# Kernel optimization log

Measured on AMD Instinct MI355X. Metric: run time of the kernel, lower is better.

The kernel has to match this reference:

```python
import jax, jax.numpy as jnp
import numpy as np

B, T_PREFIX, C_IN = 8, 6144, 8
OUT_LEN, OUT_C = 2048, 8
AUX_DIM = 16
D_MODEL, D_STATE, HEADDIM, EXPAND = 256, 32, 64, 2
D_INNER = EXPAND * D_MODEL            # 512
NHEADS = D_INNER // HEADDIM           # 8
CONV_DIM = D_INNER + 2 * D_STATE      # 576
D_PROJ = 2 * D_INNER + 2 * D_STATE + NHEADS  # 1096
N_LAYERS = 2
CHUNK = 64
PATCH = 16
PRECONV_K = 5
DCONV_K = 4


def setup_inputs() -> dict:
    key = jax.random.key(0)
    ks = iter(jax.random.split(key, 64))
    def rn(shape, s=0.02):
        return s * jax.random.normal(next(ks), shape, jnp.float32)
    inp = dict(
        x_prefix=jax.random.normal(next(ks), (B, T_PREFIX, C_IN), jnp.float32),
        y_aux=jax.random.normal(next(ks), (B, AUX_DIM), jnp.float32),
        pre_conv_w=rn((D_MODEL, C_IN, PRECONV_K), 0.1),
        pre_conv_b=rn((D_MODEL,)),
        patch_w=rn((D_MODEL, D_MODEL, PATCH), 0.05),
        patch_b=rn((D_MODEL,)),
        mask_token=rn((D_MODEL,)),
        aux_w=rn((AUX_DIM, D_MODEL), 0.1),
        aux_b=rn((D_MODEL,)),
        patch_out_w=rn((2 * D_MODEL, OUT_C * PATCH), 0.05),
        patch_out_b=rn((OUT_C * PATCH,)),
    )
    for d in ('fwd', 'bwd'):
        inp[f'{d}_norm_w'] = jnp.ones((N_LAYERS, D_MODEL), jnp.float32)
        inp[f'{d}_inproj'] = rn((N_LAYERS, D_MODEL, D_PROJ), 0.05)
        inp[f'{d}_conv_w'] = rn((N_LAYERS, CONV_DIM, DCONV_K), 0.2)
        inp[f'{d}_conv_b'] = rn((N_LAYERS, CONV_DIM))
        inp[f'{d}_dtbias'] = rn((N_LAYERS, NHEADS), 0.5)
        inp[f'{d}_Alog'] = jnp.tile(jnp.log(jnp.arange(1, NHEADS + 1, dtype=jnp.float32)), (N_LAYERS, 1))
        inp[f'{d}_D'] = jnp.ones((N_LAYERS, NHEADS), jnp.float32)
        inp[f'{d}_gnorm'] = jnp.ones((N_LAYERS, D_INNER), jnp.float32)
        inp[f'{d}_outproj'] = rn((N_LAYERS, D_INNER, D_MODEL), 0.05)
    return inp


def rmsnorm(x, w, eps=1e-5):
    return x * jax.lax.rsqrt(jnp.mean(x * x, axis=-1, keepdims=True) + eps) * w


def conv1d(x, w, b, stride, pad):  # x: [B,C,T], w: [O,I,K]
    y = jax.lax.conv_general_dilated(x, w, (stride,), [(pad, pad)],
                                     dimension_numbers=('NCH', 'OIH', 'NCH'))
    return y + b[None, :, None]


def mamba_block(u, inproj, conv_w, conv_b, dtbias, Alog, Dp, gnorm_w, outproj):
    # Mamba-2/SSD style block: in_proj -> z | xBC | dt, causal depthwise conv,
    # selective scan with per-head scalar decay A, +D skip, gated RMSNorm, out_proj.
    b, T, _ = u.shape
    zxbcdt = u @ inproj                                   # [b,T,D_PROJ]
    z = zxbcdt[..., :D_INNER]
    xBC = zxbcdt[..., D_INNER:D_INNER + CONV_DIM]
    dt = jax.nn.softplus(zxbcdt[..., -NHEADS:] + dtbias)  # [b,T,H]
    # causal depthwise conv over time
    xc = jax.lax.conv_general_dilated(xBC.transpose(0, 2, 1), conv_w[:, None, :], (1,),
                                      [(DCONV_K - 1, 0)],
                                      dimension_numbers=('NCH', 'OIH', 'NCH'),
                                      feature_group_count=CONV_DIM)
    xBC = jax.nn.silu((xc + conv_b[None, :, None]).transpose(0, 2, 1))
    xs = xBC[..., :D_INNER].reshape(b, T, NHEADS, HEADDIM)  # [b,T,H,P]
    Bm = xBC[..., D_INNER:D_INNER + D_STATE]                # [b,T,N]
    Cm = xBC[..., D_INNER + D_STATE:]                       # [b,T,N]
    A = -jnp.exp(Alog)                                      # [H]

    def step(h, inps):  # h: [b,H,P,N]
        dt_t, x_t, B_t, C_t = inps
        dA = jnp.exp(dt_t * A)[:, :, None, None]
        h = h * dA + (dt_t[:, :, None] * x_t)[..., None] * B_t[:, None, None, :]
        y = jnp.einsum('bhpn,bn->bhp', h, C_t)
        return h, y

    h0 = jnp.zeros((b, NHEADS, HEADDIM, D_STATE), u.dtype)
    _, ys = jax.lax.scan(step, h0, (dt.transpose(1, 0, 2), xs.transpose(1, 0, 2, 3),
                                    Bm.transpose(1, 0, 2), Cm.transpose(1, 0, 2)))
    y = ys.transpose(1, 0, 2, 3) + Dp[None, None, :, None] * xs
    y = y.reshape(b, T, D_INNER)
    y = rmsnorm(y * jax.nn.silu(z), gnorm_w)
    return y @ outproj


def reference(x_prefix, y_aux, pre_conv_w, pre_conv_b, patch_w, patch_b, mask_token,
              aux_w, aux_b, fwd_norm_w, fwd_inproj, fwd_conv_w, fwd_conv_b, fwd_dtbias,
              fwd_Alog, fwd_D, fwd_gnorm, fwd_outproj, bwd_norm_w, bwd_inproj,
              bwd_conv_w, bwd_conv_b, bwd_dtbias, bwd_Alog, bwd_D, bwd_gnorm,
              bwd_outproj, patch_out_w, patch_out_b):
    b = x_prefix.shape[0]
    t_total = T_PREFIX + OUT_LEN
    x_full = jnp.pad(x_prefix, ((0, 0), (0, OUT_LEN), (0, 0)))        # zeros for future
    x = jax.nn.silu(conv1d(x_full.transpose(0, 2, 1), pre_conv_w, pre_conv_b, 1, PRECONV_K // 2))
    x = conv1d(x, patch_w, patch_b, PATCH, 0).transpose(0, 2, 1)      # [b, n_tokens, d_model]
    n_tokens = x.shape[1]
    # eval mode: deterministic future-patch mask, dropout is identity
    starts = jnp.arange(n_tokens) * PATCH
    mask = (starts >= T_PREFIX)[None, :, None]
    x = jnp.where(mask, mask_token[None, None, :], x)
    aux_bias = jax.nn.silu(y_aux @ aux_w + aux_b)[:, None, :]
    x = x + aux_bias
    pad_t = (-n_tokens) % CHUNK
    if pad_t:
        x = jnp.pad(x, ((0, 0), (0, pad_t), (0, 0)))
    h_f = x
    h_b = x[:, ::-1]
    for i in range(N_LAYERS):
        h_f = h_f + mamba_block(rmsnorm(h_f, fwd_norm_w[i]), fwd_inproj[i], fwd_conv_w[i],
                                fwd_conv_b[i], fwd_dtbias[i], fwd_Alog[i], fwd_D[i],
                                fwd_gnorm[i], fwd_outproj[i])
        h_b = h_b + mamba_block(rmsnorm(h_b, bwd_norm_w[i]), bwd_inproj[i], bwd_conv_w[i],
                                bwd_conv_b[i], bwd_dtbias[i], bwd_Alog[i], bwd_D[i],
                                bwd_gnorm[i], bwd_outproj[i])
    h = jnp.concatenate([h_f, h_b[:, ::-1]], axis=-1)[:, :n_tokens]   # [b,n,2*d_model]
    patch_pred = h @ patch_out_w + patch_out_b                        # [b,n,out_c*patch]
    y = patch_pred.reshape(b, n_tokens, OUT_C, PATCH).reshape(b, n_tokens * PATCH, OUT_C)
    y = y[:, :t_total, :]
    return y[:, T_PREFIX:, :]
```

## Files before the change

kernel.cpp:

```cpp
#include <hip/hip_runtime.h>
#include <hip/hip_bf16.h>
#include <math.h>

#define BSZ      8
#define TPREF    6144
#define CIN      8
#define DMODEL   256
#define DINNER   512
#define DSTATE   32
#define NHEADS   8
#define HEADDIM  64
#define CONVDIM  576
#define DPROJ    1096
#define ZXW      1088
#define NTOK     512
#define NVIS     384
#define TBWD     128
#define MFWD     (BSZ * NTOK)
#define MBWD     (BSZ * TBWD)
#define MALL     (MFWD + MBWD)

typedef float f32x4 __attribute__((ext_vector_type(4)));
typedef __bf16 bf16x8 __attribute__((ext_vector_type(8)));

__device__ __forceinline__ float silu_f(float x) { return x / (1.f + expf(-x)); }

#define ASYNC16(gp, lp) \
    __builtin_amdgcn_global_load_lds((const __attribute__((address_space(1))) void*)(gp), \
                                     (__attribute__((address_space(3))) void*)(lp), 16, 0, 0)

__global__ __launch_bounds__(256) void gemm_mfma(
    const __bf16* __restrict__ A, const __bf16* __restrict__ Bt,
    float* __restrict__ C, const float* __restrict__ bias,
    int N, int K, int ldc, int flags) {
    __shared__ char sm[16384];
    int tid = threadIdx.x;
    int m0 = blockIdx.y * 128, n0 = blockIdx.x * 128;
    int klen = K / gridDim.z;
    int kbeg = blockIdx.z * klen;
    int w = tid >> 6, l = tid & 63;
    int wm = w >> 1, wn = w & 1;
    int lm = l & 15, q = l >> 4;

    f32x4 acc[4][4];
    #pragma unroll
    for (int i = 0; i < 4; i++)
        #pragma unroll
        for (int j = 0; j < 4; j++) acc[i][j] = (f32x4)0.f;

    for (int k0 = 0; k0 < klen; k0 += 32) {
        int kb = kbeg + k0;
        #pragma unroll
        for (int i = 0; i < 2; i++) {
            int s = i * 256 + tid;
            ASYNC16(A + (size_t)(m0 + (s >> 2)) * K + kb + (s & 3) * 8, sm + s * 16);
        }
        #pragma unroll
        for (int i = 0; i < 2; i++) {
            int s = i * 256 + tid;
            ASYNC16(Bt + (size_t)(n0 + (s >> 2)) * K + kb + (s & 3) * 8, sm + 8192 + s * 16);
        }
        __syncthreads();
        bf16x8 af[4], bfr[4];
        #pragma unroll
        for (int mf = 0; mf < 4; mf++)
            af[mf] = *(const bf16x8*)(sm + (wm * 64 + mf * 16 + lm) * 64 + q * 16);
        #pragma unroll
        for (int nf = 0; nf < 4; nf++)
            bfr[nf] = *(const bf16x8*)(sm + 8192 + (wn * 64 + nf * 16 + lm) * 64 + q * 16);
        #pragma unroll
        for (int mf = 0; mf < 4; mf++)
            #pragma unroll
            for (int nf = 0; nf < 4; nf++)
                acc[mf][nf] = __builtin_amdgcn_mfma_f32_16x16x32_bf16(af[mf], bfr[nf], acc[mf][nf], 0, 0, 0);
        __syncthreads();
    }

    #pragma unroll
    for (int mf = 0; mf < 4; mf++) {
        int mbase = m0 + wm * 64 + mf * 16 + q * 4;
        #pragma unroll
        for (int nf = 0; nf < 4; nf++) {
            int n = n0 + wn * 64 + nf * 16 + lm;
            if (n < N) {
                #pragma unroll
                for (int r = 0; r < 4; r++) {
                    float v = acc[mf][nf][r];
                    if (flags & 4) {
                        v = silu_f(v + bias[n]);
                        ((__bf16*)C)[(size_t)(mbase + r) * ldc + n] = (__bf16)v;
                    } else if (flags & 16) {
                        int mm = mbase + r;
                        int bb = mm / NVIS, tk = mm - bb * NVIS;
                        atomicAdd(C + ((size_t)(bb * NTOK + tk)) * 256 + n, v);
                    } else if (flags & 2) {
                        atomicAdd(C + (size_t)(mbase + r) * ldc + n, v);
                    } else {
                        C[(size_t)(mbase + r) * ldc + n] = v;
                    }
                }
            }
        }
    }
}

__global__ __launch_bounds__(256) void preconv_gemm(
    const float* __restrict__ xp, const __bf16* __restrict__ WpreT,
    const float* __restrict__ bias, __bf16* __restrict__ Apatch) {
    __shared__ char sm[32768];
    int tid = threadIdx.x;
    int m0 = blockIdx.y * 128, n0 = blockIdx.x * 128;
    int w = tid >> 6, l = tid & 63;
    int wm = w >> 1, wn = w & 1, lm = l & 15, q = l >> 4;

    #pragma unroll
    for (int i = 0; i < 4; i++) {
        int s = i * 256 + tid;
        int kh = s >> 9, row = (s & 511) >> 2, within = s & 3;
        ASYNC16(WpreT + (size_t)(n0 + row) * 64 + kh * 32 + within * 8, sm + 16384 + s * 16);
    }
    if (tid < 128) {
        int m = m0 + tid;
        int b = m / TPREF, t = m - b * TPREF;
        __bf16 d[64];
        #pragma unroll
        for (int j = 40; j < 64; j++) d[j] = (__bf16)0.f;
        #pragma unroll
        for (int k = 0; k < 5; k++) {
            int tt = t - 2 + k;
            bool ok = (tt >= 0) && (tt < TPREF);
            const float* s = xp + ((size_t)b * TPREF + tt) * 8;
            #pragma unroll
            for (int i = 0; i < 8; i++)
                d[i * 5 + k] = ok ? (__bf16)s[i] : (__bf16)0.f;
        }
        uint4* o0 = (uint4*)(sm + tid * 64);
        uint4* o1 = (uint4*)(sm + 8192 + tid * 64);
        #pragma unroll
        for (int k = 0; k < 4; k++) { o0[k] = ((const uint4*)d)[k]; o1[k] = ((const uint4*)d)[4 + k]; }
    }
    __syncthreads();

    f32x4 acc[4][4];
    #pragma unroll
    for (int i = 0; i < 4; i++)
        #pragma unroll
        for (int j = 0; j < 4; j++) acc[i][j] = (f32x4)0.f;
    #pragma unroll
    for (int kh = 0; kh < 2; kh++) {
        bf16x8 af[4], bfr[4];
        #pragma unroll
        for (int mf = 0; mf < 4; mf++)
            af[mf] = *(const bf16x8*)(sm + kh * 8192 + (wm * 64 + mf * 16 + lm) * 64 + q * 16);
        #pragma unroll
        for (int nf = 0; nf < 4; nf++)
            bfr[nf] = *(const bf16x8*)(sm + 16384 + kh * 8192 + (wn * 64 + nf * 16 + lm) * 64 + q * 16);
        #pragma unroll
        for (int mf = 0; mf < 4; mf++)
            #pragma unroll
            for (int nf = 0; nf < 4; nf++)
                acc[mf][nf] = __builtin_amdgcn_mfma_f32_16x16x32_bf16(af[mf], bfr[nf], acc[mf][nf], 0, 0, 0);
    }
    #pragma unroll
    for (int mf = 0; mf < 4; mf++) {
        int mbase = m0 + wm * 64 + mf * 16 + q * 4;
        #pragma unroll
        for (int nf = 0; nf < 4; nf++) {
            int n = n0 + wn * 64 + nf * 16 + lm;
            #pragma unroll
            for (int r = 0; r < 4; r++) {
                float v = silu_f(acc[mf][nf][r] + bias[n]);
                Apatch[(size_t)(mbase + r) * 256 + n] = (__bf16)v;
            }
        }
    }
}

__global__ __launch_bounds__(256) void final_gemm(
    const float* __restrict__ h_all, const __bf16* __restrict__ poT,
    float* __restrict__ out) {
    __shared__ __bf16 Asm_[128][40];
    __shared__ char Bsm[8192];
    int tid = threadIdx.x;
    int m0 = blockIdx.y * 128;
    int z = blockIdx.z;
    int dir = z >> 1, kh = z & 1;
    int koff = kh * 128;
    int w = tid >> 6, l = tid & 63;
    int wm = w >> 1, wn_ = w & 1, lm = l & 15, q = l >> 4;
    f32x4 acc[4][4];
    #pragma unroll
    for (int i = 0; i < 4; i++)
        #pragma unroll
        for (int j = 0; j < 4; j++) acc[i][j] = (f32x4)0.f;

    int r = tid >> 1, half = tid & 1;
    int m = m0 + r;
    int b = m >> 7, jj = m & 127;
    size_t arow = (dir == 0) ? ((size_t)(b * NTOK + NVIS + jj) * 256)
                             : ((size_t)MFWD * 256 + (size_t)(b * TBWD + (TBWD - 1 - jj)) * 256);
    for (int k0 = 0; k0 < 128; k0 += 32) {
        {
            const float4* sp = (const float4*)(h_all + arow + koff + k0 + half * 16);
            float4 v0 = sp[0], v1 = sp[1], v2 = sp[2], v3 = sp[3];
            union { uint4 u; __bf16 hh[8]; } d0, d1;
            d0.hh[0] = (__bf16)v0.x; d0.hh[1] = (__bf16)v0.y; d0.hh[2] = (__bf16)v0.z; d0.hh[3] = (__bf16)v0.w;
            d0.hh[4] = (__bf16)v1.x; d0.hh[5] = (__bf16)v1.y; d0.hh[6] = (__bf16)v1.z; d0.hh[7] = (__bf16)v1.w;
            d1.hh[0] = (__bf16)v2.x; d1.hh[1] = (__bf16)v2.y; d1.hh[2] = (__bf16)v2.z; d1.hh[3] = (__bf16)v2.w;
            d1.hh[4] = (__bf16)v3.x; d1.hh[5] = (__bf16)v3.y; d1.hh[6] = (__bf16)v3.z; d1.hh[7] = (__bf16)v3.w;
            *(uint4*)&Asm_[r][half * 16] = d0.u;
            *(uint4*)&Asm_[r][half * 16 + 8] = d1.u;
        }
        #pragma unroll
        for (int i = 0; i < 2; i++) {
            int s = i * 256 + tid;
            ASYNC16(poT + (size_t)(s >> 2) * 512 + dir * 256 + koff + k0 + (s & 3) * 8, Bsm + s * 16);
        }
        __syncthreads();
        bf16x8 af[4], bfr[4];
        #pragma unroll
        for (int mf = 0; mf < 4; mf++)
            af[mf] = *(const bf16x8*)&Asm_[wm * 64 + mf * 16 + lm][q * 8];
        #pragma unroll
        for (int nf = 0; nf < 4; nf++)
            bfr[nf] = *(const bf16x8*)(Bsm + (wn_ * 64 + nf * 16 + lm) * 64 + q * 16);
        #pragma unroll
        for (int mf = 0; mf < 4; mf++)
            #pragma unroll
            for (int nf = 0; nf < 4; nf++)
                acc[mf][nf] = __builtin_amdgcn_mfma_f32_16x16x32_bf16(af[mf], bfr[nf], acc[mf][nf], 0, 0, 0);
        __syncthreads();
    }
    #pragma unroll
    for (int mf = 0; mf < 4; mf++) {
        int mbase = m0 + wm * 64 + mf * 16 + q * 4;
        #pragma unroll
        for (int nf = 0; nf < 4; nf++) {
            int n = wn_ * 64 + nf * 16 + lm;
            #pragma unroll
            for (int rr = 0; rr < 4; rr++)
                atomicAdd(out + (size_t)(mbase + rr) * 128 + n, acc[mf][nf][rr]);
        }
    }
}

__global__ __launch_bounds__(256) void gemm_inproj(
    const __bf16* __restrict__ u, const __bf16* __restrict__ ipTf,
    const __bf16* __restrict__ ipTb, __bf16* __restrict__ zxb, float* __restrict__ dtc) {
    __shared__ char sm[16384];
    int tid = threadIdx.x;
    int m0 = blockIdx.y * 128, n0 = blockIdx.x * 128;
    const __bf16* Bt = (m0 >= MFWD) ? ipTb : ipTf;
    int w = tid >> 6, l = tid & 63;
    int wm = w >> 1, wn = w & 1, lm = l & 15, q = l >> 4;
    f32x4 acc[4][4];
    #pragma unroll
    for (int i = 0; i < 4; i++)
        #pragma unroll
        for (int j = 0; j < 4; j++) acc[i][j] = (f32x4)0.f;
    for (int k0 = 0; k0 < 256; k0 += 32) {
        #pragma unroll
        for (int i = 0; i < 2; i++) {
            int s = i * 256 + tid;
            ASYNC16(u + (size_t)(m0 + (s >> 2)) * 256 + k0 + (s & 3) * 8, sm + s * 16);
        }
        #pragma unroll
        for (int i = 0; i < 2; i++) {
            int s = i * 256 + tid;
            ASYNC16(Bt + (size_t)(n0 + (s >> 2)) * 256 + k0 + (s & 3) * 8, sm + 8192 + s * 16);
        }
        __syncthreads();
        bf16x8 af[4], bfr[4];
        #pragma unroll
        for (int mf = 0; mf < 4; mf++)
            af[mf] = *(const bf16x8*)(sm + (wm * 64 + mf * 16 + lm) * 64 + q * 16);
        #pragma unroll
        for (int nf = 0; nf < 4; nf++)
            bfr[nf] = *(const bf16x8*)(sm + 8192 + (wn * 64 + nf * 16 + lm) * 64 + q * 16);
        #pragma unroll
        for (int mf = 0; mf < 4; mf++)
            #pragma unroll
            for (int nf = 0; nf < 4; nf++)
                acc[mf][nf] = __builtin_amdgcn_mfma_f32_16x16x32_bf16(af[mf], bfr[nf], acc[mf][nf], 0, 0, 0);
        __syncthreads();
    }
    #pragma unroll
    for (int mf = 0; mf < 4; mf++) {
        int mbase = m0 + wm * 64 + mf * 16 + q * 4;
        #pragma unroll
        for (int nf = 0; nf < 4; nf++) {
            int n = n0 + wn * 64 + nf * 16 + lm;
            #pragma unroll
            for (int r = 0; r < 4; r++) {
                float v = acc[mf][nf][r];
                if (n < ZXW) zxb[(size_t)(mbase + r) * ZXW + n] = (__bf16)v;
                else if (n < DPROJ) dtc[(size_t)(mbase + r) * 8 + (n - ZXW)] = v;
            }
        }
    }
}

__global__ __launch_bounds__(256) void gemm_outproj(
    const __bf16* __restrict__ y2, const __bf16* __restrict__ opTf,
    const __bf16* __restrict__ opTb, float* __restrict__ C, int layer) {
    __shared__ char sm[16384];
    int tid = threadIdx.x;
    int yb = blockIdx.y;
    int m0 = (layer == 0) ? yb * 128
                          : ((yb < 8) ? (yb * 512 + 384) : (MFWD + (yb - 8) * 128));
    int n0 = blockIdx.x * 128;
    const __bf16* Bt = (m0 >= MFWD) ? opTb : opTf;
    int w = tid >> 6, l = tid & 63;
    int wm = w >> 1, wn = w & 1, lm = l & 15, q = l >> 4;
    f32x4 acc[4][4];
    #pragma unroll
    for (int i = 0; i < 4; i++)
        #pragma unroll
        for (int j = 0; j < 4; j++) acc[i][j] = (f32x4)0.f;
    for (int k0 = 0; k0 < 512; k0 += 32) {
        #pragma unroll
        for (int i = 0; i < 2; i++) {
            int s = i * 256 + tid;
            ASYNC16(y2 + (size_t)(m0 + (s >> 2)) * 512 + k0 + (s & 3) * 8, sm + s * 16);
        }
        #pragma unroll
        for (int i = 0; i < 2; i++) {
            int s = i * 256 + tid;
            ASYNC16(Bt + (size_t)(n0 + (s >> 2)) * 512 + k0 + (s & 3) * 8, sm + 8192 + s * 16);
        }
        __syncthreads();
        bf16x8 af[4], bfr[4];
        #pragma unroll
        for (int mf = 0; mf < 4; mf++)
            af[mf] = *(const bf16x8*)(sm + (wm * 64 + mf * 16 + lm) * 64 + q * 16);
        #pragma unroll
        for (int nf = 0; nf < 4; nf++)
            bfr[nf] = *(const bf16x8*)(sm + 8192 + (wn * 64 + nf * 16 + lm) * 64 + q * 16);
        #pragma unroll
        for (int mf = 0; mf < 4; mf++)
            #pragma unroll
            for (int nf = 0; nf < 4; nf++)
                acc[mf][nf] = __builtin_amdgcn_mfma_f32_16x16x32_bf16(af[mf], bfr[nf], acc[mf][nf], 0, 0, 0);
        __syncthreads();
    }
    #pragma unroll
    for (int mf = 0; mf < 4; mf++) {
        int mbase = m0 + wm * 64 + mf * 16 + q * 4;
        #pragma unroll
        for (int nf = 0; nf < 4; nf++) {
            int n = n0 + wn * 64 + nf * 16 + lm;
            #pragma unroll
            for (int r = 0; r < 4; r++) {
                size_t ci = (size_t)(mbase + r) * DMODEL + n;
                C[ci] += acc[mf][nf][r];
            }
        }
    }
}

__global__ __launch_bounds__(256) void rmsnorm_all(
    const float* __restrict__ h, const float* __restrict__ wf,
    const float* __restrict__ wb, __bf16* __restrict__ u) {
    int row = blockIdx.x * 4 + (threadIdx.x >> 6);
    int lane = threadIdx.x & 63;
    const float* w = (row >= MFWD) ? wb : wf;
    float4 v = ((const float4*)(h + (size_t)row * 256))[lane];
    float ss = v.x * v.x + v.y * v.y + v.z * v.z + v.w * v.w;
    #pragma unroll
    for (int off = 32; off >= 1; off >>= 1) ss += __shfl_xor(ss, off);
    float rs = rsqrtf(ss * (1.f / 256.f) + 1e-5f);
    float4 wv = ((const float4*)w)[lane];
    __bf16 o4[4] = {(__bf16)(v.x * rs * wv.x), (__bf16)(v.y * rs * wv.y),
                    (__bf16)(v.z * rs * wv.z), (__bf16)(v.w * rs * wv.w)};
    *(uint2*)(u + (size_t)row * 256 + lane * 4) = *(uint2*)o4;
}

__global__ __launch_bounds__(256) void gatednorm_all(
    const __bf16* __restrict__ ysD, const __bf16* __restrict__ zxb,
    const float* __restrict__ gwf, const float* __restrict__ gwb,
    __bf16* __restrict__ y2) {
    int row = blockIdx.x * 4 + (threadIdx.x >> 6);
    int lane = threadIdx.x & 63;
    const float* gw = (row >= MFWD) ? gwb : gwf;
    union { uint4 u; __bf16 hh[8]; } yv, zv;
    yv.u = *(const uint4*)(ysD + (size_t)row * 512 + lane * 8);
    zv.u = *(const uint4*)(zxb + (size_t)row * ZXW + lane * 8);
    float g[8];
    #pragma unroll
    for (int j = 0; j < 8; j++) g[j] = (float)yv.hh[j] * silu_f((float)zv.hh[j]);
    float ss = 0.f;
    #pragma unroll
    for (int j = 0; j < 8; j++) ss += g[j] * g[j];
    #pragma unroll
    for (int off = 32; off >= 1; off >>= 1) ss += __shfl_xor(ss, off);
    float rs = rsqrtf(ss * (1.f / 512.f) + 1e-5f);
    const float4* gr = (const float4*)(gw + lane * 8);
    float4 g0 = gr[0], g1 = gr[1];
    union { uint4 u; __bf16 hh[8]; } d;
    d.hh[0] = (__bf16)(g[0] * rs * g0.x); d.hh[1] = (__bf16)(g[1] * rs * g0.y);
    d.hh[2] = (__bf16)(g[2] * rs * g0.z); d.hh[3] = (__bf16)(g[3] * rs * g0.w);
    d.hh[4] = (__bf16)(g[4] * rs * g1.x); d.hh[5] = (__bf16)(g[5] * rs * g1.y);
    d.hh[6] = (__bf16)(g[6] * rs * g1.z); d.hh[7] = (__bf16)(g[7] * rs * g1.w);
    *(uint4*)(y2 + (size_t)row * 512 + lane * 8) = d.u;
}

__global__ void prep_all(const float* __restrict__ pre_conv_w, const float* __restrict__ patch_w,
                         const float* __restrict__ ip0, const float* __restrict__ ip1,
                         const float* __restrict__ op0, const float* __restrict__ op1,
                         const float* __restrict__ pow_, const float* __restrict__ pob,
                         const float* __restrict__ y_aux, const float* __restrict__ aux_w,
                         const float* __restrict__ aux_b,
                         const float* __restrict__ patch_b, const float* __restrict__ mtok,
                         __bf16* __restrict__ WpreT, __bf16* __restrict__ WtT,
                         __bf16* __restrict__ inprojT, __bf16* __restrict__ outprojT,
                         __bf16* __restrict__ poT, float* __restrict__ dout,
                         float* __restrict__ h_all) {
    __shared__ float tile[32][33];
    int bx = blockIdx.x, tid = threadIdx.x;
    int tx = tid & 31, ty = tid >> 5;
    if (bx < 256) {
        int o = bx, c = tid;
        float f[16];
        const float4* s = (const float4*)(patch_w + (size_t)o * 4096 + c * 16);
        #pragma unroll
        for (int j = 0; j < 4; j++) *(float4*)&f[j * 4] = s[j];
        #pragma unroll
        for (int k = 0; k < 16; k++)
            WtT[(size_t)o * 4096 + k * 256 + c] = (__bf16)f[k];
        return;
    }
    bx -= 256;
    if (bx < 1152) {
        int seg = bx / 288, rem = bx % 288;
        int n0 = (rem / 8) * 32, k0 = (rem % 8) * 32;
        const float* src = (seg < 2 ? ip0 : ip1) + (size_t)(seg & 1) * 256 * DPROJ;
        #pragma unroll
        for (int j = 0; j < 4; j++) {
            int r = ty + j * 8;
            int n = n0 + tx;
            tile[r][tx] = (n < DPROJ) ? src[(size_t)(k0 + r) * DPROJ + n] : 0.f;
        }
        __syncthreads();
        __bf16* dst = inprojT + (size_t)seg * 1152 * 256;
        #pragma unroll
        for (int j = 0; j < 4; j++) {
            int r = ty + j * 8;
            dst[(size_t)(n0 + r) * 256 + k0 + tx] = (__bf16)tile[tx][r];
        }
        return;
    }
    bx -= 1152;
    if (bx < 512) {
        int s = bx / 128, rem = bx % 128;
        int n0 = (rem / 16) * 32, k0 = (rem % 16) * 32;
        const float* src = (s < 2 ? op0 : op1) + (size_t)(s & 1) * DINNER * DMODEL;
        #pragma unroll
        for (int j = 0; j < 4; j++) {
            int r = ty + j * 8;
            tile[r][tx] = src[(size_t)(k0 + r) * 256 + n0 + tx];
        }
        __syncthreads();
        __bf16* dst = outprojT + (size_t)s * 256 * 512;
        #pragma unroll
        for (int j = 0; j < 4; j++) {
            int r = ty + j * 8;
            dst[(size_t)(n0 + r) * 512 + k0 + tx] = (__bf16)tile[tx][r];
        }
        return;
    }
    bx -= 512;
    if (bx < 64) {
        int n0 = (bx / 16) * 32, k0 = (bx % 16) * 32;
        #pragma unroll
        for (int j = 0; j < 4; j++) {
            int r = ty + j * 8;
            tile[r][tx] = pow_[(size_t)(k0 + r) * 128 + n0 + tx];
        }
        __syncthreads();
        #pragma unroll
        for (int j = 0; j < 4; j++) {
            int r = ty + j * 8;
            poT[(size_t)(n0 + r) * 512 + k0 + tx] = (__bf16)tile[tx][r];
        }
        return;
    }
    bx -= 64;
    if (bx < 64) {
        int idx = bx * 256 + tid;
        int o = idx >> 6, kk = idx & 63;
        WpreT[idx] = (kk < 40) ? (__bf16)pre_conv_w[o * 40 + kk] : (__bf16)0.f;
        return;
    }
    bx -= 64;
    if (bx < 512) {
        int idx = bx * 256 + tid;
        dout[idx] = pob[idx & 127];
        return;
    }
    bx -= 512;
    {
        int row = bx, o = tid;
        int b; bool masked;
        if (row < MFWD) { b = row >> 9; int tok = row & 511; masked = (tok >= NVIS); }
        else { b = (row - MFWD) >> 7; masked = true; }
        float acc = aux_b[o];
        #pragma unroll
        for (int i = 0; i < 16; i++) acc += y_aux[b * 16 + i] * aux_w[i * 256 + o];
        float v = (masked ? mtok[o] : patch_b[o]) + silu_f(acc);
        h_all[(size_t)row * 256 + o] = v;
    }
}

__global__ __launch_bounds__(256) void scan_local(
    const __bf16* __restrict__ zxb,
    const float* __restrict__ cwf, const float* __restrict__ cbf,
    const float* __restrict__ cwb, const float* __restrict__ cbb,
    const float* __restrict__ dtc,
    const float* __restrict__ dtbf, const float* __restrict__ dtbb,
    const float* __restrict__ Alogf, const float* __restrict__ Alogb,
    const float* __restrict__ Dpf, const float* __restrict__ Dpb,
    __bf16* __restrict__ ysD,
    __bf16* __restrict__ ChatF, __bf16* __restrict__ ChatB,
    float* __restrict__ dSF, float* __restrict__ dSB,
    float* __restrict__ DcsF, float* __restrict__ DcsB, int layer) {
    int id = blockIdx.x, hd = blockIdx.y;
    int b, c, T, NC; size_t rowbase;
    __bf16* Chat; float *dS, *Dcs;
    const float *dtb, *Alog, *Dp, *cw, *cb;
    if (id < 64) { b = id >> 3; c = id & 7; T = NTOK; NC = 8; rowbase = (size_t)b * NTOK;
                   Chat = ChatF; dS = dSF; Dcs = DcsF;
                   dtb = dtbf; Alog = Alogf; Dp = Dpf; cw = cwf; cb = cbf; }
    else { int i2 = id - 64; b = i2 >> 1; c = i2 & 1; T = TBWD; NC = 2;
           rowbase = (size_t)MFWD + (size_t)b * TBWD;
           Chat = ChatB; dS = dSB; Dcs = DcsB;
           dtb = dtbb; Alog = Alogb; Dp = Dpb; cw = cwb; cb = cbb; }
    bool skipY = (layer == 1) && (id < 64) && (c < 6);
    int bh = b * 8 + hd;
    int t0 = c * 64;
    int tid = threadIdx.x;
    int w = tid >> 6, l = tid & 63;
    int lm = l & 15, q = l >> 4;
    float A = -expf(Alog[hd]);
    float Dh = Dp[hd];

    __shared__ char smem[40704];
    __bf16 (*Xl)[72]  = (__bf16(*)[72])(smem);
    __bf16 (*BCl)[72] = (__bf16(*)[72])(smem + 9216);
    __bf16 (*Pl)[72]  = (__bf16(*)[72])(smem + 9216);
    __bf16 (*Wbl)[72] = (__bf16(*)[72])(smem + 18432);
    float* lcs = (float*)(smem + 23040);
    float* dts = (float*)(smem + 23296);
    __bf16 (*xraw)[64] = (__bf16(*)[64])(smem + 23552);
    __bf16 (*braw)[64] = (__bf16(*)[64])(smem + 32128);

    for (int s = tid; s < 1072; s += 256) {
        int arr = (s >= 536) ? 1 : 0;
        int s2 = s - arr * 536;
        int r = s2 >> 3, seg = s2 & 7;
        int t = t0 - 3 + r;
        uint4 v = make_uint4(0u, 0u, 0u, 0u);
        if (t >= 0) {
            size_t col = arr ? (size_t)(1024 + seg * 8) : (size_t)(DINNER + hd * 64 + seg * 8);
            v = *(const uint4*)(zxb + (rowbase + t) * (size_t)ZXW + col);
        }
        if (arr) *(uint4*)&braw[r][seg * 8] = v;
        else     *(uint4*)&xraw[r][seg * 8] = v;
    }
    __syncthreads();

    {
        int cX = hd * 64 + l;
        float w0 = cw[cX * 4], w1 = cw[cX * 4 + 1], w2 = cw[cX * 4 + 2], w3 = cw[cX * 4 + 3];
        float cbv = cb[cX];
        int tb = w * 16;
        float a0 = (float)xraw[tb][l], a1 = (float)xraw[tb + 1][l], a2 = (float)xraw[tb + 2][l];
        union { uint4 u; __bf16 h[8]; } p0, p1;
        #pragma unroll
        for (int j = 0; j < 16; j++) {
            float a3 = (float)xraw[tb + j + 3][l];
            float acc = cbv + w0 * a0 + w1 * a1 + w2 * a2 + w3 * a3;
            if (j < 8) p0.h[j] = (__bf16)silu_f(acc);
            else       p1.h[j - 8] = (__bf16)silu_f(acc);
            a0 = a1; a1 = a2; a2 = a3;
        }
        *(uint4*)&Xl[l][tb]     = p0.u;
        *(uint4*)&Xl[l][tb + 8] = p1.u;
    }
    {
        int cc = 512 + l;
        float w0 = cw[cc * 4], w1 = cw[cc * 4 + 1], w2 = cw[cc * 4 + 2], w3 = cw[cc * 4 + 3];
        float cbv = cb[cc];
        int tb = w * 16;
        float a0 = (float)braw[tb][l], a1 = (float)braw[tb + 1][l], a2 = (float)braw[tb + 2][l];
        #pragma unroll
        for (int j = 0; j < 16; j++) {
            float a3 = (float)braw[tb + j + 3][l];
            float acc = cbv + w0 * a0 + w1 * a1 + w2 * a2 + w3 * a3;
            BCl[tb + j][l] = (__bf16)silu_f(acc);
            a0 = a1; a1 = a2; a2 = a3;
        }
    }
    float xdt = dtc[(rowbase + t0 + l) * 8 + hd] + dtb[hd];
    float dtv = (xdt > 20.f) ? xdt : log1pf(expf(xdt));
    float lc = A * dtv;
    #pragma unroll
    for (int off = 1; off < 64; off <<= 1) {
        float o = __shfl_up(lc, off);
        if (l >= off) lc += o;
    }
    float lc63 = __shfl(lc, 63);
    float wj = expf(lc63 - lc) * dtv;
    float eli = expf(lc);
    if (w == 0) {
        lcs[l] = lc; dts[l] = dtv;
        if (l == 0) Dcs[bh * NC + c] = expf(lc63);
    }
    __syncthreads();

    if (!skipY) {
        union { uint4 u; __bf16 h[8]; } s, d;
        s.u = *(const uint4*)&BCl[l][32 + w * 8];
        #pragma unroll
        for (int j = 0; j < 8; j++) d.h[j] = (__bf16)(eli * (float)s.h[j]);
        *(uint4*)(Chat + ((size_t)(bh * NC + c) * 64 + l) * 32 + w * 8) = d.u;
    }
    {
        union { uint4 u; __bf16 h[8]; } s;
        s.u = *(const uint4*)&BCl[l][w * 8];
        #pragma unroll
        for (int j = 0; j < 8; j++) Wbl[w * 8 + j][l] = (__bf16)(wj * (float)s.h[j]);
    }
    bf16x8 cfr, bfr[4];
    if (!skipY) {
        cfr = *(const bf16x8*)&BCl[w * 16 + lm][32 + q * 8];
        #pragma unroll
        for (int tj = 0; tj < 4; tj++)
            if (tj <= w) bfr[tj] = *(const bf16x8*)&BCl[tj * 16 + lm][q * 8];
    }
    __syncthreads();

    if (!skipY) {
        float lci[4];
        #pragma unroll
        for (int r = 0; r < 4; r++) lci[r] = lcs[w * 16 + q * 4 + r];
        #pragma unroll
        for (int tj = 0; tj < 4; tj++) {
            if (tj > w) {
                #pragma unroll
                for (int r = 0; r < 4; r++) Pl[w * 16 + q * 4 + r][tj * 16 + lm] = (__bf16)0.f;
                continue;
            }
            f32x4 g = __builtin_amdgcn_mfma_f32_16x16x32_bf16(cfr, bfr[tj], (f32x4)0.f, 0, 0, 0);
            int j = tj * 16 + lm;
            float lcj = lcs[j], dtj = dts[j];
            #pragma unroll
            for (int r = 0; r < 4; r++) {
                int i = w * 16 + q * 4 + r;
                float v = (j <= i) ? g[r] * expf(lci[r] - lcj) * dtj : 0.f;
                if (j == i) v += Dh;
                Pl[i][j] = (__bf16)v;
            }
        }
    }
    __syncthreads();

    bf16x8 xf0[4], xf1[4];
    #pragma unroll
    for (int t4 = 0; t4 < 4; t4++) {
        xf0[t4] = *(const bf16x8*)&Xl[t4 * 16 + lm][q * 8];
        xf1[t4] = *(const bf16x8*)&Xl[t4 * 16 + lm][32 + q * 8];
    }
    if (!skipY) {
        bf16x8 pf0 = *(const bf16x8*)&Pl[w * 16 + lm][q * 8];
        bf16x8 pf1 = *(const bf16x8*)&Pl[w * 16 + lm][32 + q * 8];
        #pragma unroll
        for (int tp = 0; tp < 4; tp++) {
            f32x4 y = __builtin_amdgcn_mfma_f32_16x16x32_bf16(pf0, xf0[tp], (f32x4)0.f, 0, 0, 0);
            y = __builtin_amdgcn_mfma_f32_16x16x32_bf16(pf1, xf1[tp], y, 0, 0, 0);
            #pragma unroll
            for (int r = 0; r < 4; r++) {
                int i = w * 16 + q * 4 + r;
                ysD[(rowbase + t0 + i) * DINNER + hd * 64 + tp * 16 + lm] = (__bf16)y[r];
            }
        }
    }
    bf16x8 wf0[2], wf1[2];
    #pragma unroll
    for (int tn = 0; tn < 2; tn++) {
        wf0[tn] = *(const bf16x8*)&Wbl[tn * 16 + lm][q * 8];
        wf1[tn] = *(const bf16x8*)&Wbl[tn * 16 + lm][32 + q * 8];
    }
    float* dso = dS + (size_t)(bh * NC + c) * 2048;
    #pragma unroll
    for (int tn = 0; tn < 2; tn++) {
        f32x4 s = __builtin_amdgcn_mfma_f32_16x16x32_bf16(xf0[w], wf0[tn], (f32x4)0.f, 0, 0, 0);
        s = __builtin_amdgcn_mfma_f32_16x16x32_bf16(xf1[w], wf1[tn], s, 0, 0, 0);
        #pragma unroll
        for (int r = 0; r < 4; r++) {
            int pp = w * 16 + q * 4 + r, nn = tn * 16 + lm;
            dso[pp * 32 + nn] = s[r];
        }
    }
}

__global__ __launch_bounds__(256) void scan_tail(
    const float* __restrict__ dSF, const float* __restrict__ dSB,
    const float* __restrict__ DcsF, const float* __restrict__ DcsB,
    const __bf16* __restrict__ ChatF, const __bf16* __restrict__ ChatB,
    __bf16* __restrict__ ysD, int layer) {
    int blk = blockIdx.x;
    int dir = blk >= 64;
    int bh = blk & 63;
    int NC = dir ? 2 : 8;
    int T = dir ? TBWD : NTOK;
    int b = bh >> 3, hd = bh & 7;
    size_t rowbase = dir ? ((size_t)MFWD + (size_t)b * TBWD) : ((size_t)b * NTOK);
    const float* dS = dir ? dSB : dSF;
    const float* Dcs = dir ? DcsB : DcsF;
    const __bf16* Chat = dir ? ChatB : ChatF;
    int cmin = (layer == 1 && !dir) ? 6 : 1;
    int tid = threadIdx.x;
    __shared__ __bf16 Spl[8][64][40];
    {
        int p = tid >> 2, n0 = (tid & 3) * 8;
        float S[8];
        #pragma unroll
        for (int j = 0; j < 8; j++) S[j] = 0.f;
        for (int c = 0; c < NC; c++) {
            union { uint4 u; __bf16 hh[8]; } o;
            #pragma unroll
            for (int j = 0; j < 8; j++) o.hh[j] = (__bf16)S[j];
            *(uint4*)&Spl[c][p][n0] = o.u;
            float Dc = Dcs[bh * NC + c];
            const float4* dp = (const float4*)(dS + ((size_t)(bh * NC + c)) * 2048 + tid * 8);
            float4 d0 = dp[0], d1 = dp[1];
            S[0] = Dc * S[0] + d0.x; S[1] = Dc * S[1] + d0.y;
            S[2] = Dc * S[2] + d0.z; S[3] = Dc * S[3] + d0.w;
            S[4] = Dc * S[4] + d1.x; S[5] = Dc * S[5] + d1.y;
            S[6] = Dc * S[6] + d1.z; S[7] = Dc * S[7] + d1.w;
        }
    }
    __syncthreads();
    int w = tid >> 6, l = tid & 63, lm = l & 15, q = l >> 4;
    for (int c = cmin + w; c < NC; c += 4) {
        int t0 = c * 64;
        const __bf16* Cb = Chat + (size_t)(bh * NC + c) * 2048;
        bf16x8 cf[4], sf[4];
        #pragma unroll
        for (int t4 = 0; t4 < 4; t4++) {
            cf[t4] = *(const bf16x8*)(Cb + (t4 * 16 + lm) * 32 + q * 8);
            sf[t4] = *(const bf16x8*)&Spl[c][t4 * 16 + lm][q * 8];
        }
        #pragma unroll
        for (int ti = 0; ti < 4; ti++) {
            #pragma unroll
            for (int tp = 0; tp < 4; tp++) {
                f32x4 y = __builtin_amdgcn_mfma_f32_16x16x32_bf16(cf[ti], sf[tp], (f32x4)0.f, 0, 0, 0);
                #pragma unroll
                for (int r = 0; r < 4; r++) {
                    int i = ti * 16 + q * 4 + r;
                    size_t idx = (rowbase + t0 + i) * DINNER + hd * 64 + tp * 16 + lm;
                    ysD[idx] = (__bf16)((float)ysD[idx] + y[r]);
                }
            }
        }
    }
}

extern "C" void kernel_launch(void* const* d_in, const int* in_sizes, int n_in,
                              void* d_out, int out_size, void* d_ws, size_t ws_size,
                              hipStream_t stream) {
    const float* x_prefix    = (const float*)d_in[0];
    const float* y_aux       = (const float*)d_in[1];
    const float* pre_conv_w  = (const float*)d_in[2];
    const float* pre_conv_b  = (const float*)d_in[3];
    const float* patch_w     = (const float*)d_in[4];
    const float* patch_b     = (const float*)d_in[5];
    const float* mask_token  = (const float*)d_in[6];
    const float* aux_w       = (const float*)d_in[7];
    const float* aux_b       = (const float*)d_in[8];
    const float* patch_out_w = (const float*)d_in[9];
    const float* patch_out_b = (const float*)d_in[10];
    const float* w_norm[2]   = {(const float*)d_in[11], (const float*)d_in[20]};
    const float* w_inproj[2] = {(const float*)d_in[12], (const float*)d_in[21]};
    const float* w_convw[2]  = {(const float*)d_in[13], (const float*)d_in[22]};
    const float* w_convb[2]  = {(const float*)d_in[14], (const float*)d_in[23]};
    const float* w_dtb[2]    = {(const float*)d_in[15], (const float*)d_in[24]};
    const float* w_alog[2]   = {(const float*)d_in[16], (const float*)d_in[25]};
    const float* w_D[2]      = {(const float*)d_in[17], (const float*)d_in[26]};
    const float* w_gnorm[2]  = {(const float*)d_in[18], (const float*)d_in[27]};
    const float* w_outproj[2]= {(const float*)d_in[19], (const float*)d_in[28]};

    char* p = (char*)d_ws;
    auto alloc = [&](size_t bytes) { char* r = p; p += (bytes + 255) & ~255ULL; return r; };
    __bf16* A_patch  = (__bf16*)alloc((size_t)3072 * 4096 * 2);
    __bf16* WpreT    = (__bf16*)alloc((size_t)256 * 64 * 2);
    __bf16* WtT      = (__bf16*)alloc((size_t)256 * 4096 * 2);
    __bf16* inprojT  = (__bf16*)alloc((size_t)4 * 1152 * 256 * 2);
    __bf16* outprojT = (__bf16*)alloc((size_t)4 * 256 * 512 * 2);
    __bf16* poT      = (__bf16*)alloc((size_t)128 * 512 * 2);
    float*  h_all    = (float*)alloc((size_t)MALL * 256 * 4);
    __bf16* u        = (__bf16*)alloc((size_t)MALL * 256 * 2);
    __bf16* zxb      = (__bf16*)alloc((size_t)MALL * ZXW * 2);
    float*  dtc      = (float*)alloc((size_t)MALL * 8 * 4);
    __bf16* ysD      = (__bf16*)alloc((size_t)MALL * DINNER * 2);
    __bf16* y2       = (__bf16*)alloc((size_t)MALL * DINNER * 2);
    __bf16* ChatF    = (__bf16*)alloc((size_t)64 * 8 * 2048 * 2);
    __bf16* ChatB    = (__bf16*)alloc((size_t)64 * 2 * 2048 * 2);
    float*  dSF      = (float*)alloc((size_t)64 * 8 * 2048 * 4);
    float*  dSB      = (float*)alloc((size_t)64 * 2 * 2048 * 4);
    float*  DcsF     = (float*)alloc((size_t)64 * 8 * 4);
    float*  DcsB     = (float*)alloc((size_t)64 * 2 * 4);

    prep_all<<<256 + 1152 + 512 + 64 + 64 + 512 + MALL, 256, 0, stream>>>(
        pre_conv_w, patch_w, w_inproj[0], w_inproj[1], w_outproj[0], w_outproj[1],
        patch_out_w, patch_out_b, y_aux, aux_w, aux_b, patch_b, mask_token,
        WpreT, WtT, inprojT, outprojT, poT, (float*)d_out, h_all);
    preconv_gemm<<<dim3(2, (BSZ * TPREF) / 128), 256, 0, stream>>>(
        x_prefix, WpreT, pre_conv_b, A_patch);
    gemm_mfma<<<dim3(2, 24, 8), 256, 0, stream>>>(
        A_patch, WtT, h_all, nullptr, 256, 4096, 256, 16);

    for (int i = 0; i < 2; i++) {
        const __bf16* ipTf = inprojT + (size_t)(0 * 2 + i) * 1152 * 256;
        const __bf16* ipTb = inprojT + (size_t)(1 * 2 + i) * 1152 * 256;
        const __bf16* opTf = outprojT + (size_t)(0 * 2 + i) * 256 * 512;
        const __bf16* opTb = outprojT + (size_t)(1 * 2 + i) * 256 * 512;
        rmsnorm_all<<<MALL / 4, 256, 0, stream>>>(h_all, w_norm[0] + i * 256, w_norm[1] + i * 256, u);
        gemm_inproj<<<dim3(9, MALL / 128), 256, 0, stream>>>(u, ipTf, ipTb, zxb, dtc);
        scan_local<<<dim3(80, NHEADS), 256, 0, stream>>>(
            zxb,
            w_convw[0] + i * CONVDIM * 4, w_convb[0] + i * CONVDIM,
            w_convw[1] + i * CONVDIM * 4, w_convb[1] + i * CONVDIM,
            dtc,
            w_dtb[0] + i * 8, w_dtb[1] + i * 8,
            w_alog[0] + i * 8, w_alog[1] + i * 8,
            w_D[0] + i * 8, w_D[1] + i * 8,
            ysD, ChatF, ChatB, dSF, dSB, DcsF, DcsB, i);
        scan_tail<<<128, 256, 0, stream>>>(dSF, dSB, DcsF, DcsB, ChatF, ChatB, ysD, i);
        gatednorm_all<<<MALL / 4, 256, 0, stream>>>(
            ysD, zxb, w_gnorm[0] + i * DINNER, w_gnorm[1] + i * DINNER, y2);
        int oy = (i == 0) ? (MALL / 128) : 16;
        gemm_outproj<<<dim3(2, oy), 256, 0, stream>>>(y2, opTf, opTb, h_all, i);
    }

    final_gemm<<<dim3(1, 8, 4), 256, 0, stream>>>(h_all, poT, (float*)d_out);
}
```

Measured before the change: 323.3 us.

## Fuse RMSNorm and gated norm into in-proj and out-proj GEMM prologues

Removes the standalone rmsnorm_all and gatednorm_all kernels. Each GEMM now loads fp32 h (or ysD and z) directly, applies the weight and gating while staging the A tile into shared memory, and accumulates the row sum of squares. The per-row rsqrt scale is applied in the epilogue. This drops four launches per forward and the u/y2 intermediate round trips. The cost is that A-tile loads become synchronous register loads instead of async copies, and the norm work is redone by every column block: 9x for in-proj and 2x for out-proj.

```diff
diff --git a/kernel.cpp b/kernel.cpp
--- a/kernel.cpp
+++ b/kernel.cpp
@@ -245,12 +245,15 @@
 }
 
 __global__ __launch_bounds__(256) void gemm_inproj(
-    const __bf16* __restrict__ u, const __bf16* __restrict__ ipTf,
-    const __bf16* __restrict__ ipTb, __bf16* __restrict__ zxb, float* __restrict__ dtc) {
+    const float* __restrict__ h, const float* __restrict__ nwf, const float* __restrict__ nwb,
+    const __bf16* __restrict__ ipTf, const __bf16* __restrict__ ipTb,
+    __bf16* __restrict__ zxb, float* __restrict__ dtc) {
     __shared__ char sm[16384];
+    __shared__ float rsl[128];
     int tid = threadIdx.x;
     int m0 = blockIdx.y * 128, n0 = blockIdx.x * 128;
     const __bf16* Bt = (m0 >= MFWD) ? ipTb : ipTf;
+    const float* nw = (m0 >= MFWD) ? nwb : nwf;
     int w = tid >> 6, l = tid & 63;
     int wm = w >> 1, wn = w & 1, lm = l & 15, q = l >> 4;
     f32x4 acc[4][4];
@@ -258,11 +261,37 @@
     for (int i = 0; i < 4; i++)
         #pragma unroll
         for (int j = 0; j < 4; j++) acc[i][j] = (f32x4)0.f;
+
+    int ar = tid >> 1, aseg = tid & 1;
+    const float* hrow = h + (size_t)(m0 + ar) * 256;
+    float ss = 0.f;
+
     for (int k0 = 0; k0 < 256; k0 += 32) {
-        #pragma unroll
-        for (int i = 0; i < 2; i++) {
-            int s = i * 256 + tid;
-            ASYNC16(u + (size_t)(m0 + (s >> 2)) * 256 + k0 + (s & 3) * 8, sm + s * 16);
+        {
+            int cb = k0 + aseg * 16;
+            float4 v0 = *(const float4*)(hrow + cb);
+            float4 v1 = *(const float4*)(hrow + cb + 4);
+            float4 v2 = *(const float4*)(hrow + cb + 8);
+            float4 v3 = *(const float4*)(hrow + cb + 12);
+            float4 w0 = *(const float4*)(nw + cb);
+            float4 w1 = *(const float4*)(nw + cb + 4);
+            float4 w2 = *(const float4*)(nw + cb + 8);
+            float4 w3 = *(const float4*)(nw + cb + 12);
+            ss += v0.x * v0.x + v0.y * v0.y + v0.z * v0.z + v0.w * v0.w
+                + v1.x * v1.x + v1.y * v1.y + v1.z * v1.z + v1.w * v1.w
+                + v2.x * v2.x + v2.y * v2.y + v2.z * v2.z + v2.w * v2.w
+                + v3.x * v3.x + v3.y * v3.y + v3.z * v3.z + v3.w * v3.w;
+            union { uint4 u; __bf16 hh[8]; } d0, d1;
+            d0.hh[0] = (__bf16)(v0.x * w0.x); d0.hh[1] = (__bf16)(v0.y * w0.y);
+            d0.hh[2] = (__bf16)(v0.z * w0.z); d0.hh[3] = (__bf16)(v0.w * w0.w);
+            d0.hh[4] = (__bf16)(v1.x * w1.x); d0.hh[5] = (__bf16)(v1.y * w1.y);
+            d0.hh[6] = (__bf16)(v1.z * w1.z); d0.hh[7] = (__bf16)(v1.w * w1.w);
+            d1.hh[0] = (__bf16)(v2.x * w2.x); d1.hh[1] = (__bf16)(v2.y * w2.y);
+            d1.hh[2] = (__bf16)(v2.z * w2.z); d1.hh[3] = (__bf16)(v2.w * w2.w);
+            d1.hh[4] = (__bf16)(v3.x * w3.x); d1.hh[5] = (__bf16)(v3.y * w3.y);
+            d1.hh[6] = (__bf16)(v3.z * w3.z); d1.hh[7] = (__bf16)(v3.w * w3.w);
+            *(uint4*)(sm + ar * 64 + aseg * 32) = d0.u;
+            *(uint4*)(sm + ar * 64 + aseg * 32 + 16) = d1.u;
         }
         #pragma unroll
         for (int i = 0; i < 2; i++) {
@@ -284,15 +313,20 @@
                 acc[mf][nf] = __builtin_amdgcn_mfma_f32_16x16x32_bf16(af[mf], bfr[nf], acc[mf][nf], 0, 0, 0);
         __syncthreads();
     }
+    ss += __shfl_xor(ss, 1);
+    if (aseg == 0) rsl[ar] = rsqrtf(ss * (1.f / 256.f) + 1e-5f);
+    __syncthreads();
+
     #pragma unroll
     for (int mf = 0; mf < 4; mf++) {
-        int mbase = m0 + wm * 64 + mf * 16 + q * 4;
+        int lrow = wm * 64 + mf * 16 + q * 4;
+        int mbase = m0 + lrow;
         #pragma unroll
         for (int nf = 0; nf < 4; nf++) {
             int n = n0 + wn * 64 + nf * 16 + lm;
             #pragma unroll
             for (int r = 0; r < 4; r++) {
-                float v = acc[mf][nf][r];
+                float v = acc[mf][nf][r] * rsl[lrow + r];
                 if (n < ZXW) zxb[(size_t)(mbase + r) * ZXW + n] = (__bf16)v;
                 else if (n < DPROJ) dtc[(size_t)(mbase + r) * 8 + (n - ZXW)] = v;
             }
@@ -301,15 +335,19 @@
 }
 
 __global__ __launch_bounds__(256) void gemm_outproj(
-    const __bf16* __restrict__ y2, const __bf16* __restrict__ opTf,
-    const __bf16* __restrict__ opTb, float* __restrict__ C, int layer) {
+    const __bf16* __restrict__ ysD, const __bf16* __restrict__ zxb,
+    const float* __restrict__ gwf, const float* __restrict__ gwb,
+    const __bf16* __restrict__ opTf, const __bf16* __restrict__ opTb,
+    float* __restrict__ C, int layer) {
     __shared__ char sm[16384];
+    __shared__ float rsl[128];
     int tid = threadIdx.x;
     int yb = blockIdx.y;
     int m0 = (layer == 0) ? yb * 128
                           : ((yb < 8) ? (yb * 512 + 384) : (MFWD + (yb - 8) * 128));
     int n0 = blockIdx.x * 128;
     const __bf16* Bt = (m0 >= MFWD) ? opTb : opTf;
+    const float* gw = (m0 >= MFWD) ? gwb : gwf;
     int w = tid >> 6, l = tid & 63;
     int wm = w >> 1, wn = w & 1, lm = l & 15, q = l >> 4;
     f32x4 acc[4][4];
@@ -317,11 +355,37 @@
     for (int i = 0; i < 4; i++)
         #pragma unroll
         for (int j = 0; j < 4; j++) acc[i][j] = (f32x4)0.f;
+
+    int ar = tid >> 1, aseg = tid & 1;
+    const __bf16* yrow = ysD + (size_t)(m0 + ar) * 512;
+    const __bf16* zrow = zxb + (size_t)(m0 + ar) * ZXW;
+    float ss = 0.f;
+
     for (int k0 = 0; k0 < 512; k0 += 32) {
-        #pragma unroll
-        for (int i = 0; i < 2; i++) {
-            int s = i * 256 + tid;
-            ASYNC16(y2 + (size_t)(m0 + (s >> 2)) * 512 + k0 + (s & 3) * 8, sm + s * 16);
+        {
+            int cb = k0 + aseg * 16;
+            union { uint4 u; __bf16 hh[8]; } y0, y1, z0, z1, d0, d1;
+            y0.u = *(const uint4*)(yrow + cb);     y1.u = *(const uint4*)(yrow + cb + 8);
+            z0.u = *(const uint4*)(zrow + cb);     z1.u = *(const uint4*)(zrow + cb + 8);
+            union { float4 v[4]; float f[16]; } g;
+            g.v[0] = *(const float4*)(gw + cb);
+            g.v[1] = *(const float4*)(gw + cb + 4);
+            g.v[2] = *(const float4*)(gw + cb + 8);
+            g.v[3] = *(const float4*)(gw + cb + 12);
+            #pragma unroll
+            for (int j = 0; j < 8; j++) {
+                float x = (float)y0.hh[j] * silu_f((float)z0.hh[j]);
+                ss += x * x;
+                d0.hh[j] = (__bf16)(x * g.f[j]);
+            }
+            #pragma unroll
+            for (int j = 0; j < 8; j++) {
+                float x = (float)y1.hh[j] * silu_f((float)z1.hh[j]);
+                ss += x * x;
+                d1.hh[j] = (__bf16)(x * g.f[8 + j]);
+            }
+            *(uint4*)(sm + ar * 64 + aseg * 32) = d0.u;
+            *(uint4*)(sm + ar * 64 + aseg * 32 + 16) = d1.u;
         }
         #pragma unroll
         for (int i = 0; i < 2; i++) {
@@ -343,65 +407,24 @@
                 acc[mf][nf] = __builtin_amdgcn_mfma_f32_16x16x32_bf16(af[mf], bfr[nf], acc[mf][nf], 0, 0, 0);
         __syncthreads();
     }
+    ss += __shfl_xor(ss, 1);
+    if (aseg == 0) rsl[ar] = rsqrtf(ss * (1.f / 512.f) + 1e-5f);
+    __syncthreads();
+
     #pragma unroll
     for (int mf = 0; mf < 4; mf++) {
-        int mbase = m0 + wm * 64 + mf * 16 + q * 4;
+        int lrow = wm * 64 + mf * 16 + q * 4;
+        int mbase = m0 + lrow;
         #pragma unroll
         for (int nf = 0; nf < 4; nf++) {
             int n = n0 + wn * 64 + nf * 16 + lm;
             #pragma unroll
             for (int r = 0; r < 4; r++) {
                 size_t ci = (size_t)(mbase + r) * DMODEL + n;
-                C[ci] += acc[mf][nf][r];
-            }
-        }
-    }
-}
-
-__global__ __launch_bounds__(256) void rmsnorm_all(
-    const float* __restrict__ h, const float* __restrict__ wf,
-    const float* __restrict__ wb, __bf16* __restrict__ u) {
-    int row = blockIdx.x * 4 + (threadIdx.x >> 6);
-    int lane = threadIdx.x & 63;
-    const float* w = (row >= MFWD) ? wb : wf;
-    float4 v = ((const float4*)(h + (size_t)row * 256))[lane];
-    float ss = v.x * v.x + v.y * v.y + v.z * v.z + v.w * v.w;
-    #pragma unroll
-    for (int off = 32; off >= 1; off >>= 1) ss += __shfl_xor(ss, off);
-    float rs = rsqrtf(ss * (1.f / 256.f) + 1e-5f);
-    float4 wv = ((const float4*)w)[lane];
-    __bf16 o4[4] = {(__bf16)(v.x * rs * wv.x), (__bf16)(v.y * rs * wv.y),
-                    (__bf16)(v.z * rs * wv.z), (__bf16)(v.w * rs * wv.w)};
-    *(uint2*)(u + (size_t)row * 256 + lane * 4) = *(uint2*)o4;
-}
-
-__global__ __launch_bounds__(256) void gatednorm_all(
-    const __bf16* __restrict__ ysD, const __bf16* __restrict__ zxb,
-    const float* __restrict__ gwf, const float* __restrict__ gwb,
-    __bf16* __restrict__ y2) {
-    int row = blockIdx.x * 4 + (threadIdx.x >> 6);
-    int lane = threadIdx.x & 63;
-    const float* gw = (row >= MFWD) ? gwb : gwf;
-    union { uint4 u; __bf16 hh[8]; } yv, zv;
-    yv.u = *(const uint4*)(ysD + (size_t)row * 512 + lane * 8);
-    zv.u = *(const uint4*)(zxb + (size_t)row * ZXW + lane * 8);
-    float g[8];
-    #pragma unroll
-    for (int j = 0; j < 8; j++) g[j] = (float)yv.hh[j] * silu_f((float)zv.hh[j]);
-    float ss = 0.f;
-    #pragma unroll
-    for (int j = 0; j < 8; j++) ss += g[j] * g[j];
-    #pragma unroll
-    for (int off = 32; off >= 1; off >>= 1) ss += __shfl_xor(ss, off);
-    float rs = rsqrtf(ss * (1.f / 512.f) + 1e-5f);
-    const float4* gr = (const float4*)(gw + lane * 8);
-    float4 g0 = gr[0], g1 = gr[1];
-    union { uint4 u; __bf16 hh[8]; } d;
-    d.hh[0] = (__bf16)(g[0] * rs * g0.x); d.hh[1] = (__bf16)(g[1] * rs * g0.y);
-    d.hh[2] = (__bf16)(g[2] * rs * g0.z); d.hh[3] = (__bf16)(g[3] * rs * g0.w);
-    d.hh[4] = (__bf16)(g[4] * rs * g1.x); d.hh[5] = (__bf16)(g[5] * rs * g1.y);
-    d.hh[6] = (__bf16)(g[6] * rs * g1.z); d.hh[7] = (__bf16)(g[7] * rs * g1.w);
-    *(uint4*)(y2 + (size_t)row * 512 + lane * 8) = d.u;
+                C[ci] += acc[mf][nf][r] * rsl[lrow + r];
+            }
+        }
+    }
 }
 
 __global__ void prep_all(const float* __restrict__ pre_conv_w, const float* __restrict__ patch_w,
@@ -800,11 +823,9 @@
     __bf16* outprojT = (__bf16*)alloc((size_t)4 * 256 * 512 * 2);
     __bf16* poT      = (__bf16*)alloc((size_t)128 * 512 * 2);
     float*  h_all    = (float*)alloc((size_t)MALL * 256 * 4);
-    __bf16* u        = (__bf16*)alloc((size_t)MALL * 256 * 2);
     __bf16* zxb      = (__bf16*)alloc((size_t)MALL * ZXW * 2);
     float*  dtc      = (float*)alloc((size_t)MALL * 8 * 4);
     __bf16* ysD      = (__bf16*)alloc((size_t)MALL * DINNER * 2);
-    __bf16* y2       = (__bf16*)alloc((size_t)MALL * DINNER * 2);
     __bf16* ChatF    = (__bf16*)alloc((size_t)64 * 8 * 2048 * 2);
     __bf16* ChatB    = (__bf16*)alloc((size_t)64 * 2 * 2048 * 2);
     float*  dSF      = (float*)alloc((size_t)64 * 8 * 2048 * 4);
@@ -826,8 +847,8 @@
         const __bf16* ipTb = inprojT + (size_t)(1 * 2 + i) * 1152 * 256;
         const __bf16* opTf = outprojT + (size_t)(0 * 2 + i) * 256 * 512;
         const __bf16* opTb = outprojT + (size_t)(1 * 2 + i) * 256 * 512;
-        rmsnorm_all<<<MALL / 4, 256, 0, stream>>>(h_all, w_norm[0] + i * 256, w_norm[1] + i * 256, u);
-        gemm_inproj<<<dim3(9, MALL / 128), 256, 0, stream>>>(u, ipTf, ipTb, zxb, dtc);
+        gemm_inproj<<<dim3(9, MALL / 128), 256, 0, stream>>>(
+            h_all, w_norm[0] + i * 256, w_norm[1] + i * 256, ipTf, ipTb, zxb, dtc);
         scan_local<<<dim3(80, NHEADS), 256, 0, stream>>>(
             zxb,
             w_convw[0] + i * CONVDIM * 4, w_convb[0] + i * CONVDIM,
@@ -838,10 +859,10 @@
             w_D[0] + i * 8, w_D[1] + i * 8,
             ysD, ChatF, ChatB, dSF, dSB, DcsF, DcsB, i);
         scan_tail<<<128, 256, 0, stream>>>(dSF, dSB, DcsF, DcsB, ChatF, ChatB, ysD, i);
-        gatednorm_all<<<MALL / 4, 256, 0, stream>>>(
-            ysD, zxb, w_gnorm[0] + i * DINNER, w_gnorm[1] + i * DINNER, y2);
         int oy = (i == 0) ? (MALL / 128) : 16;
-        gemm_outproj<<<dim3(2, oy), 256, 0, stream>>>(y2, opTf, opTb, h_all, i);
+        gemm_outproj<<<dim3(2, oy), 256, 0, stream>>>(
+            ysD, zxb, w_gnorm[0] + i * DINNER, w_gnorm[1] + i * DINNER,
+            opTf, opTb, h_all, i);
     }
 
     final_gemm<<<dim3(1, 8, 4), 256, 0, stream>>>(h_all, poT, (float*)d_out);
```

Result: slower. 364.8 us (+12.9%).
